# Kernel optimization log

Measured on AMD Instinct MI355X. Metric: run time of the kernel, lower is better.

Reference implementation:

```python
import jax, jax.numpy as jnp
import numpy as np

N_STEPS = 8  # fixed-step RK4 over t in [0, 1]


def setup_inputs() -> dict:
    key = jax.random.key(0)
    ks = jax.random.split(key, 5)
    B, T, F, C = 64, 4096, 76, 15
    x = jax.random.normal(ks[0], (B, T, F), dtype=jnp.float32)
    # Conv1d(76->76, k=3) weights, PyTorch OIH layout, fan-in scaled
    conv_w = jax.random.normal(ks[1], (F, F, 3), dtype=jnp.float32) * (1.0 / np.sqrt(F * 3))
    conv_b = jax.random.normal(ks[2], (F,), dtype=jnp.float32) * 0.01
    final_w = jax.random.normal(ks[3], (C, F), dtype=jnp.float32) * (1.0 / np.sqrt(F))
    final_b = jax.random.normal(ks[4], (C,), dtype=jnp.float32) * 0.01
    return {"x": x, "conv_w": conv_w, "conv_b": conv_b,
            "final_w": final_w, "final_b": final_b}


def _func(h, conv_w, conv_b):
    # h: [B, F, T]; Conv1d k=3 pad=1 -> Tanh (the ODE vector field)
    y = jax.lax.conv_general_dilated(
        h, conv_w, window_strides=(1,), padding=[(1, 1)],
        dimension_numbers=("NCH", "OIH", "NCH"))
    return jnp.tanh(y + conv_b[None, :, None])


def reference(x, conv_w, conv_b, final_w, final_b):
    # x: [B, T, F] -> permute to channels-first for Conv1d
    h0 = jnp.transpose(x, (0, 2, 1))  # [B, F, T]
    dt = jnp.float32(1.0 / N_STEPS)

    def rk4_step(h, _):
        k1 = _func(h, conv_w, conv_b)
        k2 = _func(h + 0.5 * dt * k1, conv_w, conv_b)
        k3 = _func(h + 0.5 * dt * k2, conv_w, conv_b)
        k4 = _func(h + dt * k3, conv_w, conv_b)
        return h + (dt / 6.0) * (k1 + 2.0 * k2 + 2.0 * k3 + k4), None

    hT, _ = jax.lax.scan(rk4_step, h0, None, length=N_STEPS)
    # back to [B, T, F], then final Linear(F -> num_classes)
    out = jnp.einsum("bft,cf->btc", hT, final_w) + final_b
    return out
```

## Files before the change

kernel.cpp:

```cpp
#include <hip/hip_runtime.h>
#include <cstdint>
#include <cstddef>

#define F_CH 76
#define T_LEN 4096
#define B_TOT 64
#define C_CLS 15
#define NSTEP 8

#define W_OUT  112
#define HALO2  8
#define NBT    37
#define NKB    5
#define WSTR   88
#define SST    128
#define SROWS  130
#define TPB    768
#define HP     80

#define C2LOG2E 2.8853900817779268f

typedef __attribute__((ext_vector_type(8)))  __bf16 bf16x8;
typedef __attribute__((ext_vector_type(4)))  __bf16 bf16x4;
typedef __attribute__((ext_vector_type(16))) float  f32x16;

__device__ __forceinline__ int sw_off(int r, int v) {
    return r * SST + (((v) ^ (r & 7)) << 3);
}

__global__ __launch_bounds__(256) void pad_copy_kernel(
    const float* __restrict__ x, float* __restrict__ h, int b0)
{
    int bl = blockIdx.y;
    int q  = blockIdx.x * 256 + threadIdx.x;
    int t  = q / 20, c4 = (q - t * 20) * 4;
    float4 v = {0.f, 0.f, 0.f, 0.f};
    if (c4 < F_CH)
        v = *(const float4*)(x + ((size_t)(b0 + bl) * T_LEN + t) * F_CH + c4);
    *(float4*)(h + ((size_t)bl * T_LEN + t) * HP + c4) = v;
}

__global__ __launch_bounds__(256) void wprep_kernel(
    const float* __restrict__ cw, __bf16* __restrict__ wpb)
{
    int idx = blockIdx.x * 256 + threadIdx.x;
    if (idx >= 3 * 96 * WSTR) return;
    int tap = idx / (96 * WSTR);
    int rem = idx - tap * 96 * WSTR;
    int c = rem / WSTR, ci = rem - c * WSTR;
    float v = 0.0f;
    if (c < F_CH && ci < F_CH) v = cw[((size_t)c * F_CH + ci) * 3 + tap];
    wpb[idx] = (__bf16)v;
}

__global__ __launch_bounds__(TPB, 3) void rk4_step2_kernel(
    const float* __restrict__ hin, float* __restrict__ hout,
    const __bf16* __restrict__ wpb, const float* __restrict__ cb)
{
    __shared__ __bf16 s_lds[2][SROWS * SST];
    __shared__ float  cb_lds[96];

    const int b    = blockIdx.y;
    const int T0   = blockIdx.x * W_OUT;
    const int tid  = threadIdx.x;
    const int lane = tid & 63;
    const int l31  = lane & 31;
    const int l5   = lane >> 5;
    const int wv   = tid >> 6;
    const int ct   = wv >> 2;
    const int tq   = wv & 3;

    const int  rb  = tq * 32 + l31;
    const int  tg  = T0 - HALO2 + rb;
    const bool tok = (tg >= 0 && tg < T_LEN);

    if (tid < 256) {
        int bi = tid / 128, rr = (tid % 128) / 64, c = tid % 64;
        ((uint32_t*)&s_lds[bi][(rr ? (SROWS - 1) : 0) * SST])[c] = 0u;
    }
    if (tid < 96) cb_lds[tid] = (tid < F_CH) ? cb[tid] * C2LOG2E : 0.0f;

    float  hn[16];
    bf16x4 hpk[4];
    const float* hb = hin + (size_t)b * T_LEN * HP;
    #pragma unroll
    for (int q = 0; q < 4; ++q) {
        int c0 = ct * 32 + l5 * 4 + q * 8;
        float4 v = {0.f, 0.f, 0.f, 0.f};
        if (tok && c0 < HP) v = *(const float4*)(hb + (size_t)tg * HP + c0);
        hn[q*4+0]=v.x; hn[q*4+1]=v.y; hn[q*4+2]=v.z; hn[q*4+3]=v.w;
        hpk[q][0]=(__bf16)v.x; hpk[q][1]=(__bf16)v.y;
        hpk[q][2]=(__bf16)v.z; hpk[q][3]=(__bf16)v.w;
    }

    bf16x8 afr[3][NKB];
    #pragma unroll
    for (int tap = 0; tap < 3; ++tap)
        #pragma unroll
        for (int kb = 0; kb < NKB; ++kb)
            afr[tap][kb] = *(const bf16x8*)&wpb[((size_t)tap * 96 + ct * 32 + l31) * WSTR
                                                + kb * 16 + l5 * 8];

    const float dt = 0.125f;

    #pragma unroll 1
    for (int st = 0; st < 2; ++st) {
        #pragma unroll
        for (int q = 0; q < 4; ++q) {
            int c0 = ct * 32 + l5 * 4 + q * 8;
            if (c0 < HP)
                *(bf16x4*)&s_lds[0][sw_off(rb + 1, ct * 4 + q) + l5 * 4] = hpk[q];
        }
        __syncthreads();

        #pragma unroll 1
        for (int e = 0; e < 4; ++e) {
            const float we   = (e == 0 || e == 3) ? dt / 6.0f : dt / 3.0f;
            const float al   = (e == 2) ? dt : 0.5f * dt;
            const float al_t = tok ? al : 0.0f;

            const __bf16* sb = s_lds[e & 1];
            f32x16 a0 = {};
            #pragma unroll
            for (int tap = 0; tap < 3; ++tap) {
                #pragma unroll
                for (int kb = 0; kb < NKB; ++kb) {
                    bf16x8 bf = *(const bf16x8*)&sb[sw_off(rb + tap, kb * 2 + l5)];
                    a0 = __builtin_amdgcn_mfma_f32_32x32x16_bf16(afr[tap][kb], bf, a0, 0, 0, 0);
                }
            }

            __bf16* sw = s_lds[(e + 1) & 1];
            #pragma unroll
            for (int q = 0; q < 4; ++q) {
                int c0 = ct * 32 + l5 * 4 + q * 8;
                if (c0 >= HP) continue;
                bf16x4 p;
                #pragma unroll
                for (int j = 0; j < 4; ++j) {
                    float y  = fmaf(a0[q*4+j], C2LOG2E, cb_lds[c0 + j]);
                    float ex = __builtin_amdgcn_exp2f(y);
                    float kv = fmaf(-2.0f, __builtin_amdgcn_rcpf(ex + 1.0f), 1.0f);
                    hn[q*4+j] = fmaf(we, kv, hn[q*4+j]);
                    if (e < 3) p[j] = (__bf16)fmaf(al_t, kv, (float)hpk[q][j]);
                }
                if (e < 3)
                    *(bf16x4*)&sw[sw_off(rb + 1, ct * 4 + q) + l5 * 4] = p;
            }
            if (e < 3) __syncthreads();
        }

        if (st == 0) {
            #pragma unroll
            for (int i = 0; i < 16; ++i) hn[i] = tok ? hn[i] : 0.0f;
            #pragma unroll
            for (int q = 0; q < 4; ++q)
                #pragma unroll
                for (int j = 0; j < 4; ++j) hpk[q][j] = (__bf16)hn[q*4+j];
            __syncthreads();
        }
    }

    if (rb >= HALO2 && rb < HALO2 + W_OUT && tg < T_LEN) {
        float* ho = hout + ((size_t)b * T_LEN + tg) * HP;
        #pragma unroll
        for (int q = 0; q < 4; ++q) {
            int c0 = ct * 32 + l5 * 4 + q * 8;
            if (c0 < HP) {
                float4 v;
                v.x = hn[q*4+0]; v.y = hn[q*4+1];
                v.z = hn[q*4+2]; v.w = hn[q*4+3];
                *(float4*)(ho + c0) = v;
            }
        }
    }
}

__global__ __launch_bounds__(256) void final_kernel(
    const float* __restrict__ h, const float* __restrict__ fw,
    const float* __restrict__ fb, float* __restrict__ out, int b0)
{
    int bl = blockIdx.y;
    int t  = blockIdx.x * 256 + threadIdx.x;
    const float* hr = h + ((size_t)bl * T_LEN + t) * HP;
    float acc[C_CLS];
#pragma unroll
    for (int c = 0; c < C_CLS; ++c) acc[c] = fb[c];
#pragma unroll
    for (int qf = 0; qf < 19; ++qf) {
        float4 v = *(const float4*)(hr + qf * 4);
#pragma unroll
        for (int c = 0; c < C_CLS; ++c) {
            const float* w = fw + c * F_CH + qf * 4;
            acc[c] = fmaf(w[0], v.x, acc[c]);
            acc[c] = fmaf(w[1], v.y, acc[c]);
            acc[c] = fmaf(w[2], v.z, acc[c]);
            acc[c] = fmaf(w[3], v.w, acc[c]);
        }
    }
    float* ob = out + ((size_t)(b0 + bl) * T_LEN + t) * C_CLS;
#pragma unroll
    for (int c = 0; c < C_CLS; ++c) ob[c] = acc[c];
}

extern "C" void kernel_launch(void* const* d_in, const int* in_sizes, int n_in,
                              void* d_out, int out_size, void* d_ws, size_t ws_size,
                              hipStream_t stream)
{
    const float* x  = (const float*)d_in[0];
    const float* cw = (const float*)d_in[1];
    const float* cb = (const float*)d_in[2];
    const float* fw = (const float*)d_in[3];
    const float* fb = (const float*)d_in[4];
    float* out = (float*)d_out;

    const size_t FT = (size_t)T_LEN * HP;

    __bf16* WPB = (__bf16*)d_ws;
    const size_t wpbFloats = 12800;
    float* planes = (float*)d_ws + wpbFloats;

    size_t planeBytes = 2 * FT * sizeof(float);
    size_t avail = ws_size - wpbFloats * sizeof(float);
    int Bc = (int)(avail / planeBytes);
    if (Bc > B_TOT) Bc = B_TOT;
    if (Bc < 1) Bc = 1;

    float* H0 = planes;
    float* H1 = H0 + (size_t)Bc * FT;

    wprep_kernel<<<(3 * 96 * WSTR + 255) / 256, 256, 0, stream>>>(cw, WPB);

    for (int b0 = 0; b0 < B_TOT; b0 += Bc) {
        int bc = (B_TOT - b0 < Bc) ? (B_TOT - b0) : Bc;

        dim3 gP(T_LEN * 20 / 256, bc);
        pad_copy_kernel<<<gP, 256, 0, stream>>>(x, H0, b0);

        float* hcur = H0;
        float* hnxt = H1;
        dim3 gR(NBT, bc);
        for (int st2 = 0; st2 < NSTEP / 2; ++st2) {
            rk4_step2_kernel<<<gR, TPB, 0, stream>>>(hcur, hnxt, WPB, cb);
            float* tmp = hcur; hcur = hnxt; hnxt = tmp;
        }

        dim3 gF(T_LEN / 256, bc);
        final_kernel<<<gF, 256, 0, stream>>>(hcur, fw, fb, out, b0);
    }
}
```

Baseline: 818.0 us.

## Split fused two-step RK4 kernel into single-step kernel with small time tiles

Replaces the kernel that fused two RK4 steps over 112-wide time tiles (768 threads, halo 8) with one RK4 step per launch over 24-wide tiles (192 threads, halo 4). This gives many more, smaller blocks for occupancy and less register and LDS pressure. The conv bias is now loaded into registers and used to initialise the MFMA accumulator, replacing the LDS bias table and the extra FMA. In exchange it launches twice as many step kernels, doubles the global reads and writes of the state, and spends a larger fraction of MFMA work on halo rows.

New measurement: 2.046 ms. +150.1%, slower.

```diff
diff --git a/kernel.cpp b/kernel.cpp
--- a/kernel.cpp
+++ b/kernel.cpp
@@ -8,14 +8,14 @@
 #define C_CLS 15
 #define NSTEP 8
 
-#define W_OUT  112
-#define HALO2  8
-#define NBT    37
+#define W_OUT  24
+#define HALO   4
+#define NBT    171
 #define NKB    5
 #define WSTR   88
 #define SST    128
-#define SROWS  130
-#define TPB    768
+#define SROWS  34
+#define TPB    192
 #define HP     80
 
 #define C2LOG2E 2.8853900817779268f
@@ -53,12 +53,11 @@
     wpb[idx] = (__bf16)v;
 }
 
-__global__ __launch_bounds__(TPB, 3) void rk4_step2_kernel(
+__global__ __launch_bounds__(TPB, 4) void rk4_step_kernel(
     const float* __restrict__ hin, float* __restrict__ hout,
     const __bf16* __restrict__ wpb, const float* __restrict__ cb)
 {
     __shared__ __bf16 s_lds[2][SROWS * SST];
-    __shared__ float  cb_lds[96];
 
     const int b    = blockIdx.y;
     const int T0   = blockIdx.x * W_OUT;
@@ -66,19 +65,22 @@
     const int lane = tid & 63;
     const int l31  = lane & 31;
     const int l5   = lane >> 5;
-    const int wv   = tid >> 6;
-    const int ct   = wv >> 2;
-    const int tq   = wv & 3;
-
-    const int  rb  = tq * 32 + l31;
-    const int  tg  = T0 - HALO2 + rb;
+    const int ct   = tid >> 6;
+
+    const int  rb  = l31;
+    const int  tg  = T0 - HALO + rb;
     const bool tok = (tg >= 0 && tg < T_LEN);
 
-    if (tid < 256) {
-        int bi = tid / 128, rr = (tid % 128) / 64, c = tid % 64;
+    {
+        int i0 = tid;
+        int i1 = tid + 192;
+        int bi = i0 >> 7, rr = (i0 >> 6) & 1, c = i0 & 63;
         ((uint32_t*)&s_lds[bi][(rr ? (SROWS - 1) : 0) * SST])[c] = 0u;
-    }
-    if (tid < 96) cb_lds[tid] = (tid < F_CH) ? cb[tid] * C2LOG2E : 0.0f;
+        if (i1 < 256) {
+            int bj = i1 >> 7, rs = (i1 >> 6) & 1, d = i1 & 63;
+            ((uint32_t*)&s_lds[bj][(rs ? (SROWS - 1) : 0) * SST])[d] = 0u;
+        }
+    }
 
     float  hn[16];
     bf16x4 hpk[4];
@@ -93,6 +95,15 @@
         hpk[q][2]=(__bf16)v.z; hpk[q][3]=(__bf16)v.w;
     }
 
+    float cbs[16];
+    #pragma unroll
+    for (int q = 0; q < 4; ++q)
+        #pragma unroll
+        for (int j = 0; j < 4; ++j) {
+            int c = ct * 32 + l5 * 4 + q * 8 + j;
+            cbs[q*4+j] = (c < F_CH) ? cb[c] : 0.0f;
+        }
+
     bf16x8 afr[3][NKB];
     #pragma unroll
     for (int tap = 0; tap < 3; ++tap)
@@ -101,67 +112,56 @@
             afr[tap][kb] = *(const bf16x8*)&wpb[((size_t)tap * 96 + ct * 32 + l31) * WSTR
                                                 + kb * 16 + l5 * 8];
 
+    #pragma unroll
+    for (int q = 0; q < 4; ++q) {
+        int c0 = ct * 32 + l5 * 4 + q * 8;
+        if (c0 < HP)
+            *(bf16x4*)&s_lds[0][sw_off(rb + 1, ct * 4 + q) + l5 * 4] = hpk[q];
+    }
+
     const float dt = 0.125f;
 
     #pragma unroll 1
-    for (int st = 0; st < 2; ++st) {
+    for (int e = 0; e < 4; ++e) {
+        const float we   = (e == 0 || e == 3) ? dt / 6.0f : dt / 3.0f;
+        const float al   = (e == 2) ? dt : 0.5f * dt;
+        const float al_t = tok ? al : 0.0f;
+
+        __syncthreads();
+
+        const __bf16* sb = s_lds[e & 1];
+        f32x16 a0;
+        #pragma unroll
+        for (int i = 0; i < 16; ++i) a0[i] = cbs[i];
+        #pragma unroll
+        for (int tap = 0; tap < 3; ++tap) {
+            #pragma unroll
+            for (int kb = 0; kb < NKB; ++kb) {
+                bf16x8 bf = *(const bf16x8*)&sb[sw_off(rb + tap, kb * 2 + l5)];
+                a0 = __builtin_amdgcn_mfma_f32_32x32x16_bf16(afr[tap][kb], bf, a0, 0, 0, 0);
+            }
+        }
+
+        __bf16* sw = s_lds[(e + 1) & 1];
         #pragma unroll
         for (int q = 0; q < 4; ++q) {
             int c0 = ct * 32 + l5 * 4 + q * 8;
-            if (c0 < HP)
-                *(bf16x4*)&s_lds[0][sw_off(rb + 1, ct * 4 + q) + l5 * 4] = hpk[q];
-        }
-        __syncthreads();
-
-        #pragma unroll 1
-        for (int e = 0; e < 4; ++e) {
-            const float we   = (e == 0 || e == 3) ? dt / 6.0f : dt / 3.0f;
-            const float al   = (e == 2) ? dt : 0.5f * dt;
-            const float al_t = tok ? al : 0.0f;
-
-            const __bf16* sb = s_lds[e & 1];
-            f32x16 a0 = {};
+            if (c0 >= HP) continue;
+            bf16x4 p;
             #pragma unroll
-            for (int tap = 0; tap < 3; ++tap) {
-                #pragma unroll
-                for (int kb = 0; kb < NKB; ++kb) {
-                    bf16x8 bf = *(const bf16x8*)&sb[sw_off(rb + tap, kb * 2 + l5)];
-                    a0 = __builtin_amdgcn_mfma_f32_32x32x16_bf16(afr[tap][kb], bf, a0, 0, 0, 0);
-                }
+            for (int j = 0; j < 4; ++j) {
+                float y  = a0[q*4+j] * C2LOG2E;
+                float ex = __builtin_amdgcn_exp2f(y);
+                float kv = fmaf(-2.0f, __builtin_amdgcn_rcpf(ex + 1.0f), 1.0f);
+                hn[q*4+j] = fmaf(we, kv, hn[q*4+j]);
+                if (e < 3) p[j] = (__bf16)fmaf(al_t, kv, (float)hpk[q][j]);
             }
-
-            __bf16* sw = s_lds[(e + 1) & 1];
-            #pragma unroll
-            for (int q = 0; q < 4; ++q) {
-                int c0 = ct * 32 + l5 * 4 + q * 8;
-                if (c0 >= HP) continue;
-                bf16x4 p;
-                #pragma unroll
-                for (int j = 0; j < 4; ++j) {
-                    float y  = fmaf(a0[q*4+j], C2LOG2E, cb_lds[c0 + j]);
-                    float ex = __builtin_amdgcn_exp2f(y);
-                    float kv = fmaf(-2.0f, __builtin_amdgcn_rcpf(ex + 1.0f), 1.0f);
-                    hn[q*4+j] = fmaf(we, kv, hn[q*4+j]);
-                    if (e < 3) p[j] = (__bf16)fmaf(al_t, kv, (float)hpk[q][j]);
-                }
-                if (e < 3)
-                    *(bf16x4*)&sw[sw_off(rb + 1, ct * 4 + q) + l5 * 4] = p;
-            }
-            if (e < 3) __syncthreads();
-        }
-
-        if (st == 0) {
-            #pragma unroll
-            for (int i = 0; i < 16; ++i) hn[i] = tok ? hn[i] : 0.0f;
-            #pragma unroll
-            for (int q = 0; q < 4; ++q)
-                #pragma unroll
-                for (int j = 0; j < 4; ++j) hpk[q][j] = (__bf16)hn[q*4+j];
-            __syncthreads();
-        }
-    }
-
-    if (rb >= HALO2 && rb < HALO2 + W_OUT && tg < T_LEN) {
+            if (e < 3)
+                *(bf16x4*)&sw[sw_off(rb + 1, ct * 4 + q) + l5 * 4] = p;
+        }
+    }
+
+    if (rb >= HALO && rb < HALO + W_OUT && tg < T_LEN) {
         float* ho = hout + ((size_t)b * T_LEN + tg) * HP;
         #pragma unroll
         for (int q = 0; q < 4; ++q) {
@@ -240,8 +240,8 @@
         float* hcur = H0;
         float* hnxt = H1;
         dim3 gR(NBT, bc);
-        for (int st2 = 0; st2 < NSTEP / 2; ++st2) {
-            rk4_step2_kernel<<<gR, TPB, 0, stream>>>(hcur, hnxt, WPB, cb);
+        for (int st = 0; st < NSTEP; ++st) {
+            rk4_step_kernel<<<gR, TPB, 0, stream>>>(hcur, hnxt, WPB, cb);
             float* tmp = hcur; hcur = hnxt; hnxt = tmp;
         }
 
```
